# Kernel optimization log

Measured on AMD Instinct MI355X. Metric: run time of the kernel, lower is better.

Reference implementation:

```python
import jax, jax.numpy as jnp
import numpy as np

KT = 1.0

def l2norm(x, eps=1e-12):
    # torch F.normalize(p=2): x / max(||x||, eps)
    n = jnp.sqrt(jnp.sum(x * x, axis=-1, keepdims=True))
    return x / jnp.maximum(n, eps)

def setup_inputs() -> dict:
    key = jax.random.key(0)
    k1, k2, k3 = jax.random.split(key, 3)
    B, T, key_dim, e_dim, n_e = 16, 1024, 256, 256, 512
    key_soft = jax.random.normal(k1, (B, T, key_dim), dtype=jnp.float32)
    # embedding tables init uniform(-1/n_e, 1/n_e) as in the torch module
    keys = jax.random.uniform(k2, (n_e, key_dim), minval=-1.0 / n_e, maxval=1.0 / n_e, dtype=jnp.float32)
    vparams = jax.random.uniform(k3, (n_e, e_dim), minval=-1.0 / n_e, maxval=1.0 / n_e, dtype=jnp.float32)
    return {"key_soft": key_soft, "keys": keys, "vparams": vparams}

def reference(key_soft, keys, vparams):
    # clustering_forward of VQClassifierNN
    ksn = l2norm(key_soft)                                  # [B,T,D]
    keys_norm = l2norm(keys)                                # [n_e,D]
    score_ksh = jnp.einsum('btd,nd->btn', ksn, keys_norm)   # [B,T,n_e]
    score_kss = jnp.einsum('btd,bsd->bts', ksn, ksn)        # [B,T,T]
    # softmax weighting over codebook (score_to_weight)
    w = jax.nn.softmax(score_ksh / KT, axis=-1)
    w = jnp.nan_to_num(w)
    vp_norm = l2norm(vparams)                               # [n_e,E]
    vparams_w = l2norm(jnp.einsum('btn,ne->bte', w, vp_norm))  # [B,T,E]
    score_vpss = jnp.einsum('bte,bse->bts', vparams_w, vparams_w)  # [B,T,T]
    score_vpsh = jnp.einsum('bte,ne->btn', vparams_w, vp_norm)     # [B,T,n_e]
    encoding_indices = jnp.argmax(score_ksh, axis=-1)       # [B,T] int
    vparams_hard = l2norm(vparams[encoding_indices])        # gather + normalize
    # straight-through: grads flow through vparams_w
    vparams_hard = vparams_w + jax.lax.stop_gradient(vparams_hard - vparams_w)
    return (encoding_indices, vparams_w, vparams_hard,
            score_vpss, score_vpsh, score_kss, score_ksh)
```

## Files before the change

### kernel.cpp

```cpp
#include <hip/hip_runtime.h>
#include <hip/hip_bf16.h>

#define BB 16
#define TT 1024
#define DD 256
#define NE 512
#define BT 16384

typedef unsigned short ushort_t;
typedef __attribute__((ext_vector_type(8))) short bf16x8;
typedef __attribute__((ext_vector_type(4))) float f32x4;

#define AS_GLOBAL __attribute__((address_space(1)))
#define AS_SHARED __attribute__((address_space(3)))

static __device__ __forceinline__ ushort_t f2bf(float f) {
    union { float f; unsigned u; } x; x.f = f;
    unsigned r = x.u + 0x7fffu + ((x.u >> 16) & 1u);
    return (ushort_t)(r >> 16);
}

__global__ __launch_bounds__(256) void l2norm_dual(const float* __restrict__ in,
                                                   float* __restrict__ out,
                                                   ushort_t* __restrict__ out_bf) {
    const int row = blockIdx.x;
    const long long base = (long long)row * DD;
    const int t = threadIdx.x;
    float v = in[base + t];
    float ss = v * v;
    #pragma unroll
    for (int off = 32; off > 0; off >>= 1) ss += __shfl_down(ss, off, 64);
    __shared__ float partial[4];
    const int wave = t >> 6, lane = t & 63;
    if (lane == 0) partial[wave] = ss;
    __syncthreads();
    __shared__ float s_inv;
    if (t == 0) {
        float tot = partial[0] + partial[1] + partial[2] + partial[3];
        s_inv = 1.0f / fmaxf(sqrtf(tot), 1e-12f);
    }
    __syncthreads();
    const float r = v * s_inv;
    out[base + t] = r;
    if (out_bf) out_bf[base + t] = f2bf(r);
}

__global__ void transpose_bf(const float* __restrict__ in, ushort_t* __restrict__ out,
                             int rows, int cols) {
    int idx = blockIdx.x * blockDim.x + threadIdx.x;
    if (idx < rows * cols) {
        int r = idx / cols, c = idx - r * cols;
        out[(long long)c * rows + r] = f2bf(in[idx]);
    }
}

__global__ __launch_bounds__(256) void gemm_bf16_nt(const ushort_t* __restrict__ A,
                                                    const ushort_t* __restrict__ Bm,
                                                    float* __restrict__ C,
                                                    int M, int N, int K,
                                                    long long sA, long long sB, long long sC) {
    A  += sA * blockIdx.z;
    Bm += sB * blockIdx.z;
    C  += sC * blockIdx.z;
    const int bm = blockIdx.y * 128;
    const int bn = blockIdx.x * 128;

    __shared__ ushort_t As[128 * 32];
    __shared__ ushort_t Bs[128 * 32];

    const int tid = threadIdx.x;
    const int wv = tid >> 6;
    const int ln = tid & 63;

    const int srow   = ln >> 2;
    const int schunk = (ln & 3) * 8;

    const int wm = (wv >> 1) * 64;
    const int wn = (wv & 1) * 64;
    const int fr = ln & 15;
    const int fq = (ln >> 4) * 8;

    f32x4 acc[4][4] = {};

    for (int k0 = 0; k0 < K; k0 += 32) {
        #pragma unroll
        for (int t = 0; t < 2; ++t) {
            const int ra = wv * 32 + t * 16;
            const ushort_t* ga = A + (long long)(bm + ra + srow) * K + k0 + schunk;
            __builtin_amdgcn_global_load_lds((const AS_GLOBAL void*)ga,
                                             (AS_SHARED void*)&As[ra * 32], 16, 0, 0);
            const ushort_t* gb = Bm + (long long)(bn + ra + srow) * K + k0 + schunk;
            __builtin_amdgcn_global_load_lds((const AS_GLOBAL void*)gb,
                                             (AS_SHARED void*)&Bs[ra * 32], 16, 0, 0);
        }
        __syncthreads();

        bf16x8 af[4], bfr[4];
        #pragma unroll
        for (int i = 0; i < 4; ++i)
            af[i] = *(const bf16x8*)&As[(wm + i * 16 + fr) * 32 + fq];
        #pragma unroll
        for (int j = 0; j < 4; ++j)
            bfr[j] = *(const bf16x8*)&Bs[(wn + j * 16 + fr) * 32 + fq];
        #pragma unroll
        for (int i = 0; i < 4; ++i)
            #pragma unroll
            for (int j = 0; j < 4; ++j)
                acc[i][j] = __builtin_amdgcn_mfma_f32_16x16x32_bf16(af[i], bfr[j], acc[i][j], 0, 0, 0);
        __syncthreads();
    }

    const int col  = ln & 15;
    const int qrow = (ln >> 4) * 4;
    #pragma unroll
    for (int i = 0; i < 4; ++i)
        #pragma unroll
        for (int j = 0; j < 4; ++j) {
            #pragma unroll
            for (int r = 0; r < 4; ++r)
                C[(long long)(bm + wm + i * 16 + qrow + r) * N + bn + wn + j * 16 + col] = acc[i][j][r];
        }
}

__global__ __launch_bounds__(256) void softmax_argmax(const float* __restrict__ S,
                                                      const float* __restrict__ ks_raw,
                                                      const float* __restrict__ keys_raw,
                                                      float* __restrict__ idx_out,
                                                      ushort_t* __restrict__ W) {
    const int row = blockIdx.x;
    const long long base = (long long)row * NE;
    const int t = threadIdx.x;
    const float v0 = S[base + t];
    const float v1 = S[base + t + 256];

    float bv = fmaxf(v0, v1);
    #pragma unroll
    for (int off = 32; off > 0; off >>= 1) bv = fmaxf(bv, __shfl_down(bv, off, 64));
    __shared__ float pv[4];
    const int wave = t >> 6, lane = t & 63;
    if (lane == 0) pv[wave] = bv;
    __syncthreads();
    __shared__ float s_max;
    if (t == 0) s_max = fmaxf(fmaxf(pv[0], pv[1]), fmaxf(pv[2], pv[3]));
    __syncthreads();
    const float m = s_max;

    __shared__ int cand[128];
    __shared__ int ncand;
    if (t == 0) ncand = 0;
    __syncthreads();
    const float DELTA = 0.02f;
    if (v0 >= m - DELTA) { int p = atomicAdd(&ncand, 1); if (p < 128) cand[p] = t; }
    if (v1 >= m - DELTA) { int p = atomicAdd(&ncand, 1); if (p < 128) cand[p] = t + 256; }
    __syncthreads();
    const int nc = min(ncand, 128);

    __shared__ double wbv[4];
    __shared__ int    wbi[4];
    {
        double best = -1e300; int besti = 0x7fffffff;
        const float* arow = ks_raw + (long long)row * DD;
        const double a0 = (double)arow[lane];
        const double a1 = (double)arow[lane + 64];
        const double a2 = (double)arow[lane + 128];
        const double a3 = (double)arow[lane + 192];
        for (int k = wave; k < nc; k += 4) {
            const int c = cand[k];
            const float* krow = keys_raw + (long long)c * DD;
            const double b0 = (double)krow[lane];
            const double b1 = (double)krow[lane + 64];
            const double b2 = (double)krow[lane + 128];
            const double b3 = (double)krow[lane + 192];
            double dp = a0 * b0 + a1 * b1 + a2 * b2 + a3 * b3;
            double nb = b0 * b0 + b1 * b1 + b2 * b2 + b3 * b3;
            #pragma unroll
            for (int off = 32; off > 0; off >>= 1) {
                dp += __shfl_down(dp, off, 64);
                nb += __shfl_down(nb, off, 64);
            }
            dp = __shfl(dp, 0, 64);
            nb = __shfl(nb, 0, 64);
            const double d = dp / sqrt(nb);
            if (d > best || (d == best && c < besti)) { best = d; besti = c; }
        }
        if (lane == 0) { wbv[wave] = best; wbi[wave] = besti; }
    }
    __syncthreads();
    if (t == 0) {
        double best = wbv[0]; int besti = wbi[0];
        #pragma unroll
        for (int k = 1; k < 4; ++k)
            if (wbv[k] > best || (wbv[k] == best && wbi[k] < besti)) { best = wbv[k]; besti = wbi[k]; }
        idx_out[row] = (float)besti;
    }

    const float e0 = expf(v0 - m);
    const float e1 = expf(v1 - m);
    float ssum = e0 + e1;
    #pragma unroll
    for (int off = 32; off > 0; off >>= 1) ssum += __shfl_down(ssum, off, 64);
    __shared__ float ps[4];
    if (lane == 0) ps[wave] = ssum;
    __syncthreads();
    __shared__ float s_sum;
    if (t == 0) s_sum = ps[0] + ps[1] + ps[2] + ps[3];
    __syncthreads();
    const float inv = 1.0f / s_sum;
    W[base + t]       = f2bf(e0 * inv);
    W[base + t + 256] = f2bf(e1 * inv);
}

__global__ __launch_bounds__(256) void vpw_finish(const float* __restrict__ raw,
                                                  const float* __restrict__ idxf,
                                                  const float* __restrict__ vp_norm,
                                                  float* __restrict__ vpw,
                                                  ushort_t* __restrict__ vpw_bf,
                                                  float* __restrict__ vph) {
    const int row = blockIdx.x;
    const long long base = (long long)row * DD;
    const int t = threadIdx.x;
    const float v = raw[base + t];
    float ss = v * v;
    #pragma unroll
    for (int off = 32; off > 0; off >>= 1) ss += __shfl_down(ss, off, 64);
    __shared__ float partial[4];
    const int wave = t >> 6, lane = t & 63;
    if (lane == 0) partial[wave] = ss;
    __syncthreads();
    __shared__ float s_inv;
    if (t == 0) {
        float tot = partial[0] + partial[1] + partial[2] + partial[3];
        s_inv = 1.0f / fmaxf(sqrtf(tot), 1e-12f);
    }
    __syncthreads();
    const float r = v * s_inv;
    vpw[base + t] = r;
    vpw_bf[base + t] = f2bf(r);
    const int idx = (int)idxf[row];
    vph[base + t] = vp_norm[(long long)idx * DD + t];
}

extern "C" void kernel_launch(void* const* d_in, const int* in_sizes, int n_in,
                              void* d_out, int out_size, void* d_ws, size_t ws_size,
                              hipStream_t stream) {
    const float* key_soft = (const float*)d_in[0];
    const float* keys     = (const float*)d_in[1];
    const float* vparams  = (const float*)d_in[2];
    float* out = (float*)d_out;

    const long long off0 = 0;
    const long long off1 = off0 + BT;
    const long long off2 = off1 + (long long)BT * DD;
    const long long off3 = off2 + (long long)BT * DD;
    const long long off4 = off3 + (long long)BB * TT * TT;
    const long long off5 = off4 + (long long)BT * NE;
    const long long off6 = off5 + (long long)BB * TT * TT;

    float* o_idx  = out + off0;
    float* o_vpw  = out + off1;
    float* o_vph  = out + off2;
    float* o_vpss = out + off3;
    float* o_vpsh = out + off4;
    float* o_kss  = out + off5;
    float* o_ksh  = out + off6;

    float*    keys_n    = (float*)d_ws;
    float*    vp_n      = keys_n + (long long)NE * DD;
    ushort_t* vp_n_bf   = (ushort_t*)(vp_n + (long long)NE * DD);
    ushort_t* vpnT_bf   = vp_n_bf + (long long)NE * DD;
    ushort_t* vpw_bf    = vpnT_bf + (long long)DD * NE;
    ushort_t* keys_n_bf = vpw_bf + (long long)BT * DD;

    float*    ksn     = o_kss;
    ushort_t* ksn_bf  = (ushort_t*)o_vpsh;
    float*    raw_scr = o_vpss;
    ushort_t* w_bf    = (ushort_t*)(o_vpss + (long long)BT * DD);

    l2norm_dual<<<BT, 256, 0, stream>>>(key_soft, ksn, ksn_bf);
    l2norm_dual<<<NE, 256, 0, stream>>>(keys, keys_n, keys_n_bf);
    l2norm_dual<<<NE, 256, 0, stream>>>(vparams, vp_n, vp_n_bf);
    transpose_bf<<<(NE * DD + 255) / 256, 256, 0, stream>>>(vp_n, vpnT_bf, NE, DD);

    gemm_bf16_nt<<<dim3(NE / 128, BT / 128, 1), 256, 0, stream>>>(
        ksn_bf, keys_n_bf, o_ksh, BT, NE, DD, 0, 0, 0);

    softmax_argmax<<<BT, 256, 0, stream>>>(o_ksh, key_soft, keys, o_idx, w_bf);

    gemm_bf16_nt<<<dim3(DD / 128, BT / 128, 1), 256, 0, stream>>>(
        w_bf, vpnT_bf, raw_scr, BT, DD, NE, 0, 0, 0);

    gemm_bf16_nt<<<dim3(TT / 128, TT / 128, BB), 256, 0, stream>>>(
        ksn_bf, ksn_bf, o_kss, TT, TT, DD,
        (long long)TT * DD, (long long)TT * DD, (long long)TT * TT);

    vpw_finish<<<BT, 256, 0, stream>>>(raw_scr, o_idx, vp_n, o_vpw, vpw_bf, o_vph);

    gemm_bf16_nt<<<dim3(TT / 128, TT / 128, BB), 256, 0, stream>>>(
        vpw_bf, vpw_bf, o_vpss, TT, TT, DD,
        (long long)TT * DD, (long long)TT * DD, (long long)TT * TT);

    gemm_bf16_nt<<<dim3(NE / 128, BT / 128, 1), 256, 0, stream>>>(
        vpw_bf, vp_n_bf, o_vpsh, BT, NE, DD, 0, 0, 0);
}
```

Measured before the change: 362.1 us.

## Fuse prep kernels, batch GEMMs into mega launches, fuse vpw GEMM with normalization

Merges the three l2norm launches and the transpose into one prep kernel, which writes only the bf16 outputs needed and vectorizes the key_soft path. It also combines the kss batched GEMM with the ksh GEMM, and the vpss GEMM with the vpsh GEMM, into two single launches with 1536 blocks each. The w×vp GEMM now computes row L2 norms in its epilogue and does the hard-gather, which removes the fp32 scratch round trip and the separate finish kernel. The costs are a specialized fixed-K GEMM and a fused GEMM tile that is narrower in M, with 64 rows per block.

```diff
diff --git a/kernel.cpp b/kernel.cpp
--- a/kernel.cpp
+++ b/kernel.cpp
@@ -20,50 +20,83 @@
     return (ushort_t)(r >> 16);
 }
 
-__global__ __launch_bounds__(256) void l2norm_dual(const float* __restrict__ in,
-                                                   float* __restrict__ out,
-                                                   ushort_t* __restrict__ out_bf) {
-    const int row = blockIdx.x;
-    const long long base = (long long)row * DD;
+__global__ __launch_bounds__(256) void prep_all(const float* __restrict__ ks,
+                                                const float* __restrict__ keys,
+                                                const float* __restrict__ vparams,
+                                                ushort_t* __restrict__ ksn_bf,
+                                                ushort_t* __restrict__ keys_n_bf,
+                                                float* __restrict__ vp_n,
+                                                ushort_t* __restrict__ vp_n_bf,
+                                                ushort_t* __restrict__ vpnT_bf) {
+    const int bid = blockIdx.x;
     const int t = threadIdx.x;
-    float v = in[base + t];
-    float ss = v * v;
-    #pragma unroll
-    for (int off = 32; off > 0; off >>= 1) ss += __shfl_down(ss, off, 64);
-    __shared__ float partial[4];
-    const int wave = t >> 6, lane = t & 63;
-    if (lane == 0) partial[wave] = ss;
-    __syncthreads();
-    __shared__ float s_inv;
-    if (t == 0) {
-        float tot = partial[0] + partial[1] + partial[2] + partial[3];
-        s_inv = 1.0f / fmaxf(sqrtf(tot), 1e-12f);
-    }
-    __syncthreads();
-    const float r = v * s_inv;
-    out[base + t] = r;
-    if (out_bf) out_bf[base + t] = f2bf(r);
-}
-
-__global__ void transpose_bf(const float* __restrict__ in, ushort_t* __restrict__ out,
-                             int rows, int cols) {
-    int idx = blockIdx.x * blockDim.x + threadIdx.x;
-    if (idx < rows * cols) {
-        int r = idx / cols, c = idx - r * cols;
-        out[(long long)c * rows + r] = f2bf(in[idx]);
-    }
-}
-
-__global__ __launch_bounds__(256) void gemm_bf16_nt(const ushort_t* __restrict__ A,
-                                                    const ushort_t* __restrict__ Bm,
-                                                    float* __restrict__ C,
-                                                    int M, int N, int K,
-                                                    long long sA, long long sB, long long sC) {
-    A  += sA * blockIdx.z;
-    Bm += sB * blockIdx.z;
-    C  += sC * blockIdx.z;
-    const int bm = blockIdx.y * 128;
-    const int bn = blockIdx.x * 128;
+    if (bid < 4096) {
+        const int row  = bid * 4 + (t >> 6);
+        const int lane = t & 63;
+        const float4 v = *(const float4*)(ks + (long long)row * DD + lane * 4);
+        float ss = v.x * v.x + v.y * v.y + v.z * v.z + v.w * v.w;
+        #pragma unroll
+        for (int off = 32; off > 0; off >>= 1) ss += __shfl_down(ss, off, 64);
+        ss = __shfl(ss, 0, 64);
+        const float inv = 1.0f / fmaxf(sqrtf(ss), 1e-12f);
+        unsigned long long p =
+              (unsigned long long)f2bf(v.x * inv)
+            | ((unsigned long long)f2bf(v.y * inv) << 16)
+            | ((unsigned long long)f2bf(v.z * inv) << 32)
+            | ((unsigned long long)f2bf(v.w * inv) << 48);
+        *(unsigned long long*)(ksn_bf + (long long)row * DD + lane * 4) = p;
+    } else {
+        const int b2 = bid - 4096;
+        const bool is_keys = (b2 < NE);
+        const int rr = is_keys ? b2 : b2 - NE;
+        const float* src = (is_keys ? keys : vparams) + (long long)rr * DD;
+        const float v = src[t];
+        float ss = v * v;
+        #pragma unroll
+        for (int off = 32; off > 0; off >>= 1) ss += __shfl_down(ss, off, 64);
+        __shared__ float partial[4];
+        const int wave = t >> 6, lane = t & 63;
+        if (lane == 0) partial[wave] = ss;
+        __syncthreads();
+        __shared__ float s_inv;
+        if (t == 0) {
+            float tot = partial[0] + partial[1] + partial[2] + partial[3];
+            s_inv = 1.0f / fmaxf(sqrtf(tot), 1e-12f);
+        }
+        __syncthreads();
+        const float r = v * s_inv;
+        const ushort_t b = f2bf(r);
+        if (is_keys) {
+            keys_n_bf[(long long)rr * DD + t] = b;
+        } else {
+            vp_n[(long long)rr * DD + t] = r;
+            vp_n_bf[(long long)rr * DD + t] = b;
+            vpnT_bf[(long long)t * NE + rr] = b;
+        }
+    }
+}
+
+__global__ __launch_bounds__(256) void mega_gemm(const ushort_t* __restrict__ Ab,
+                                                 const ushort_t* __restrict__ Bb,
+                                                 float* __restrict__ Cb,
+                                                 const ushort_t* __restrict__ Af,
+                                                 const ushort_t* __restrict__ Bf,
+                                                 float* __restrict__ Cf) {
+    const int bid = blockIdx.x;
+    const ushort_t *A, *Bm;
+    float* C;
+    int bm, bn, ldc;
+    if (bid < 1024) {
+        const int z = bid >> 6, t6 = bid & 63;
+        A  = Ab + (long long)z * TT * DD;
+        Bm = Bb + (long long)z * TT * DD;
+        C  = Cb + (long long)z * TT * TT;
+        bm = (t6 >> 3) * 128; bn = (t6 & 7) * 128; ldc = TT;
+    } else {
+        const int f = bid - 1024;
+        A = Af; Bm = Bf; C = Cf;
+        bm = (f >> 2) * 128; bn = (f & 3) * 128; ldc = NE;
+    }
 
     __shared__ ushort_t As[128 * 32];
     __shared__ ushort_t Bs[128 * 32];
@@ -71,10 +104,8 @@
     const int tid = threadIdx.x;
     const int wv = tid >> 6;
     const int ln = tid & 63;
-
     const int srow   = ln >> 2;
     const int schunk = (ln & 3) * 8;
-
     const int wm = (wv >> 1) * 64;
     const int wn = (wv & 1) * 64;
     const int fr = ln & 15;
@@ -82,14 +113,14 @@
 
     f32x4 acc[4][4] = {};
 
-    for (int k0 = 0; k0 < K; k0 += 32) {
+    for (int k0 = 0; k0 < DD; k0 += 32) {
         #pragma unroll
         for (int t = 0; t < 2; ++t) {
             const int ra = wv * 32 + t * 16;
-            const ushort_t* ga = A + (long long)(bm + ra + srow) * K + k0 + schunk;
+            const ushort_t* ga = A + (long long)(bm + ra + srow) * DD + k0 + schunk;
             __builtin_amdgcn_global_load_lds((const AS_GLOBAL void*)ga,
                                              (AS_SHARED void*)&As[ra * 32], 16, 0, 0);
-            const ushort_t* gb = Bm + (long long)(bn + ra + srow) * K + k0 + schunk;
+            const ushort_t* gb = Bm + (long long)(bn + ra + srow) * DD + k0 + schunk;
             __builtin_amdgcn_global_load_lds((const AS_GLOBAL void*)gb,
                                              (AS_SHARED void*)&Bs[ra * 32], 16, 0, 0);
         }
@@ -115,11 +146,10 @@
     #pragma unroll
     for (int i = 0; i < 4; ++i)
         #pragma unroll
-        for (int j = 0; j < 4; ++j) {
+        for (int j = 0; j < 4; ++j)
             #pragma unroll
             for (int r = 0; r < 4; ++r)
-                C[(long long)(bm + wm + i * 16 + qrow + r) * N + bn + wn + j * 16 + col] = acc[i][j][r];
-        }
+                C[(long long)(bm + wm + i * 16 + qrow + r) * ldc + bn + wn + j * 16 + col] = acc[i][j][r];
 }
 
 __global__ __launch_bounds__(256) void softmax_argmax(const float* __restrict__ S,
@@ -210,34 +240,105 @@
     W[base + t + 256] = f2bf(e1 * inv);
 }
 
-__global__ __launch_bounds__(256) void vpw_finish(const float* __restrict__ raw,
-                                                  const float* __restrict__ idxf,
-                                                  const float* __restrict__ vp_norm,
-                                                  float* __restrict__ vpw,
-                                                  ushort_t* __restrict__ vpw_bf,
-                                                  float* __restrict__ vph) {
-    const int row = blockIdx.x;
-    const long long base = (long long)row * DD;
-    const int t = threadIdx.x;
-    const float v = raw[base + t];
-    float ss = v * v;
-    #pragma unroll
-    for (int off = 32; off > 0; off >>= 1) ss += __shfl_down(ss, off, 64);
-    __shared__ float partial[4];
-    const int wave = t >> 6, lane = t & 63;
-    if (lane == 0) partial[wave] = ss;
-    __syncthreads();
-    __shared__ float s_inv;
-    if (t == 0) {
-        float tot = partial[0] + partial[1] + partial[2] + partial[3];
-        s_inv = 1.0f / fmaxf(sqrtf(tot), 1e-12f);
-    }
-    __syncthreads();
-    const float r = v * s_inv;
-    vpw[base + t] = r;
-    vpw_bf[base + t] = f2bf(r);
-    const int idx = (int)idxf[row];
-    vph[base + t] = vp_norm[(long long)idx * DD + t];
+__global__ __launch_bounds__(256) void gemm_vpw_norm(const ushort_t* __restrict__ Aw,
+                                                     const ushort_t* __restrict__ BvT,
+                                                     const float* __restrict__ idxf,
+                                                     const float* __restrict__ vp_n,
+                                                     float* __restrict__ vpw,
+                                                     ushort_t* __restrict__ vpw_bf,
+                                                     float* __restrict__ vph) {
+    const int bm = blockIdx.x * 64;
+
+    __shared__ ushort_t As[64 * 32];
+    __shared__ ushort_t Bs[256 * 32];
+
+    const int tid = threadIdx.x;
+    const int wv = tid >> 6;
+    const int ln = tid & 63;
+    const int srow   = ln >> 2;
+    const int schunk = (ln & 3) * 8;
+    const int wn = wv * 64;
+    const int fr = ln & 15;
+    const int fq = (ln >> 4) * 8;
+
+    f32x4 acc[4][4] = {};
+
+    for (int k0 = 0; k0 < NE; k0 += 32) {
+        #pragma unroll
+        for (int s = 0; s < 5; ++s) {
+            const int g = wv * 5 + s;
+            if (g < 4) {
+                const ushort_t* ga = Aw + (long long)(bm + g * 16 + srow) * NE + k0 + schunk;
+                __builtin_amdgcn_global_load_lds((const AS_GLOBAL void*)ga,
+                                                 (AS_SHARED void*)&As[(g * 16) * 32], 16, 0, 0);
+            } else {
+                const int rb = (g - 4) * 16;
+                const ushort_t* gb = BvT + (long long)(rb + srow) * NE + k0 + schunk;
+                __builtin_amdgcn_global_load_lds((const AS_GLOBAL void*)gb,
+                                                 (AS_SHARED void*)&Bs[rb * 32], 16, 0, 0);
+            }
+        }
+        __syncthreads();
+
+        bf16x8 af[4], bfr[4];
+        #pragma unroll
+        for (int i = 0; i < 4; ++i)
+            af[i] = *(const bf16x8*)&As[(i * 16 + fr) * 32 + fq];
+        #pragma unroll
+        for (int j = 0; j < 4; ++j)
+            bfr[j] = *(const bf16x8*)&Bs[(wn + j * 16 + fr) * 32 + fq];
+        #pragma unroll
+        for (int i = 0; i < 4; ++i)
+            #pragma unroll
+            for (int j = 0; j < 4; ++j)
+                acc[i][j] = __builtin_amdgcn_mfma_f32_16x16x32_bf16(af[i], bfr[j], acc[i][j], 0, 0, 0);
+        __syncthreads();
+    }
+
+    __shared__ float sq[64][4];
+    __shared__ float inv_s[64];
+    __shared__ int   sidx[64];
+    const int qrow = (ln >> 4) * 4;
+    #pragma unroll
+    for (int i = 0; i < 4; ++i) {
+        #pragma unroll
+        for (int r = 0; r < 4; ++r) {
+            float s = 0.0f;
+            #pragma unroll
+            for (int j = 0; j < 4; ++j) { const float a = acc[i][j][r]; s += a * a; }
+            #pragma unroll
+            for (int msk = 1; msk < 16; msk <<= 1) s += __shfl_xor(s, msk, 64);
+            if ((ln & 15) == 0) sq[i * 16 + qrow + r][wv] = s;
+        }
+    }
+    if (tid < 64) sidx[tid] = (int)idxf[bm + tid];
+    __syncthreads();
+    if (tid < 64) {
+        const float tot = sq[tid][0] + sq[tid][1] + sq[tid][2] + sq[tid][3];
+        inv_s[tid] = 1.0f / fmaxf(sqrtf(tot), 1e-12f);
+    }
+    __syncthreads();
+
+    const int col = ln & 15;
+    #pragma unroll
+    for (int i = 0; i < 4; ++i)
+        #pragma unroll
+        for (int r = 0; r < 4; ++r) {
+            const int row = i * 16 + qrow + r;
+            const float iv = inv_s[row];
+            #pragma unroll
+            for (int j = 0; j < 4; ++j) {
+                const float v = acc[i][j][r] * iv;
+                const long long o = (long long)(bm + row) * DD + wn + j * 16 + col;
+                vpw[o] = v;
+                vpw_bf[o] = f2bf(v);
+            }
+        }
+
+    for (int k = 0; k < 64; ++k) {
+        const int grow = bm + k;
+        vph[(long long)grow * DD + tid] = vp_n[(long long)sidx[k] * DD + tid];
+    }
 }
 
 extern "C" void kernel_launch(void* const* d_in, const int* in_sizes, int n_in,
@@ -264,41 +365,26 @@
     float* o_kss  = out + off5;
     float* o_ksh  = out + off6;
 
-    float*    keys_n    = (float*)d_ws;
-    float*    vp_n      = keys_n + (long long)NE * DD;
+    float*    vp_n      = (float*)d_ws;
     ushort_t* vp_n_bf   = (ushort_t*)(vp_n + (long long)NE * DD);
     ushort_t* vpnT_bf   = vp_n_bf + (long long)NE * DD;
     ushort_t* vpw_bf    = vpnT_bf + (long long)DD * NE;
     ushort_t* keys_n_bf = vpw_bf + (long long)BT * DD;
 
-    float*    ksn     = o_kss;
-    ushort_t* ksn_bf  = (ushort_t*)o_vpsh;
-    float*    raw_scr = o_vpss;
-    ushort_t* w_bf    = (ushort_t*)(o_vpss + (long long)BT * DD);
-
-    l2norm_dual<<<BT, 256, 0, stream>>>(key_soft, ksn, ksn_bf);
-    l2norm_dual<<<NE, 256, 0, stream>>>(keys, keys_n, keys_n_bf);
-    l2norm_dual<<<NE, 256, 0, stream>>>(vparams, vp_n, vp_n_bf);
-    transpose_bf<<<(NE * DD + 255) / 256, 256, 0, stream>>>(vp_n, vpnT_bf, NE, DD);
-
-    gemm_bf16_nt<<<dim3(NE / 128, BT / 128, 1), 256, 0, stream>>>(
-        ksn_bf, keys_n_bf, o_ksh, BT, NE, DD, 0, 0, 0);
+    ushort_t* ksn_bf = (ushort_t*)o_vpsh;
+    ushort_t* w_bf   = (ushort_t*)(o_vpss + (long long)BT * DD);
+
+    prep_all<<<4096 + 2 * NE, 256, 0, stream>>>(
+        key_soft, keys, vparams, ksn_bf, keys_n_bf, vp_n, vp_n_bf, vpnT_bf);
+
+    mega_gemm<<<1536, 256, 0, stream>>>(
+        ksn_bf, ksn_bf, o_kss, ksn_bf, keys_n_bf, o_ksh);
 
     softmax_argmax<<<BT, 256, 0, stream>>>(o_ksh, key_soft, keys, o_idx, w_bf);
 
-    gemm_bf16_nt<<<dim3(DD / 128, BT / 128, 1), 256, 0, stream>>>(
-        w_bf, vpnT_bf, raw_scr, BT, DD, NE, 0, 0, 0);
-
-    gemm_bf16_nt<<<dim3(TT / 128, TT / 128, BB), 256, 0, stream>>>(
-        ksn_bf, ksn_bf, o_kss, TT, TT, DD,
-        (long long)TT * DD, (long long)TT * DD, (long long)TT * TT);
-
-    vpw_finish<<<BT, 256, 0, stream>>>(raw_scr, o_idx, vp_n, o_vpw, vpw_bf, o_vph);
-
-    gemm_bf16_nt<<<dim3(TT / 128, TT / 128, BB), 256, 0, stream>>>(
-        vpw_bf, vpw_bf, o_vpss, TT, TT, DD,
-        (long long)TT * DD, (long long)TT * DD, (long long)TT * TT);
-
-    gemm_bf16_nt<<<dim3(NE / 128, BT / 128, 1), 256, 0, stream>>>(
-        vpw_bf, vp_n_bf, o_vpsh, BT, NE, DD, 0, 0, 0);
-}
+    gemm_vpw_norm<<<BT / 64, 256, 0, stream>>>(
+        w_bf, vpnT_bf, o_idx, vp_n, o_vpw, vpw_bf, o_vph);
+
+    mega_gemm<<<1536, 256, 0, stream>>>(
+        vpw_bf, vpw_bf, o_vpss, vpw_bf, vp_n_bf, o_vpsh);
+}
```

Result: faster. 325.6 us (-10.1%).
